# Kernel optimization log

Hardware: AMD Instinct MI355X
Metric: run time of the kernel (lower is better)

## Reference

```python
import jax, jax.numpy as jnp
import numpy as np

N_HEADS = 4
NUM_GROUPS = 32
EPS = 1e-6


def _nin(t, W, b):
    # 1x1 conv as dense over channel dim: [B,C,H,W] x [C,D] -> [B,D,H,W]
    return jnp.einsum('bchw,cd->bdhw', t, W) + b[None, :, None, None]


def setup_inputs() -> dict:
    key = jax.random.key(0)
    ks = jax.random.split(key, 12)
    B, C, H, W = 8, 256, 32, 32
    Tc = 512
    Cin = C + Tc  # 768
    x = jax.random.normal(ks[0], (B, C, H, W), dtype=jnp.float32)
    text_feat = jax.random.normal(ks[1], (B, Tc), dtype=jnp.float32)
    gn_gamma = jnp.ones((Cin,), dtype=jnp.float32)
    gn_beta = jnp.zeros((Cin,), dtype=jnp.float32)
    scale = 1.0 / np.sqrt(Cin)
    W0 = jax.random.normal(ks[2], (Cin, C), dtype=jnp.float32) * scale
    b0 = jnp.zeros((C,), dtype=jnp.float32)
    W1 = jax.random.normal(ks[3], (Cin, C), dtype=jnp.float32) * scale
    b1 = jnp.zeros((C,), dtype=jnp.float32)
    W2 = jax.random.normal(ks[4], (Cin, C), dtype=jnp.float32) * scale
    b2 = jnp.zeros((C,), dtype=jnp.float32)
    return {"x": x, "text_feat": text_feat, "gn_gamma": gn_gamma, "gn_beta": gn_beta,
            "W0": W0, "b0": b0, "W1": W1, "b1": b1, "W2": W2, "b2": b2}


def reference(x, text_feat, gn_gamma, gn_beta, W0, b0, W1, b1, W2, b2):
    B, C, H, W = x.shape
    # broadcast text features spatially and concat on channel dim
    tf = jnp.broadcast_to(text_feat[:, :, None, None], (B, text_feat.shape[1], H, W))
    h = jnp.concatenate([x, tf], axis=1)  # [B, C+Tc, H, W]
    Ctot = h.shape[1]
    # GroupNorm(32, Ctot), eps=1e-6
    hg = h.reshape(B, NUM_GROUPS, Ctot // NUM_GROUPS, H, W)
    mu = hg.mean(axis=(2, 3, 4), keepdims=True)
    var = hg.var(axis=(2, 3, 4), keepdims=True)
    hn = ((hg - mu) * jax.lax.rsqrt(var + EPS)).reshape(B, Ctot, H, W)
    hn = hn * gn_gamma[None, :, None, None] + gn_beta[None, :, None, None]
    q = _nin(hn, W0, b0)
    k = _nin(hn, W1, b1)
    v = _nin(hn, W2, b2)
    Ch = C // N_HEADS
    qh = q.reshape(B * N_HEADS, Ch, H, W)
    kh = k.reshape(B * N_HEADS, Ch, H, W)
    vh = v.reshape(B * N_HEADS, Ch, H, W)
    # full HW x HW attention scores, softmax over flattened key positions
    w = jnp.einsum('bchw,bcij->bhwij', qh, kh) * (Ch ** -0.5)
    w = jax.nn.softmax(w.reshape(B * N_HEADS, H, W, H * W), axis=-1)
    w = w.reshape(B * N_HEADS, H, W, H, W)
    ho = jnp.einsum('bhwij,bcij->bchw', w, vh).reshape(B, C, H, W)
    return x + ho
```

## Files before the change

kernel.cpp:

```cpp
#include <hip/hip_runtime.h>
#include <math.h>

#define BATCH 8
#define CX 256
#define TC 512
#define CIN 768
#define HW_TOT 1024
#define NH 4
#define CHD 64

typedef __attribute__((ext_vector_type(8))) short short8;
typedef __attribute__((ext_vector_type(4))) short s4v;
typedef __attribute__((ext_vector_type(4))) float floatx4;
typedef __attribute__((ext_vector_type(4))) int int4v;

#define QSCALE 0.18033688f

static __device__ __forceinline__ short f2bf(float f) {
    union { float f; unsigned u; } c; c.f = f;
    unsigned r = (c.u + 0x7fffu + ((c.u >> 16) & 1u)) >> 16;
    return (short)r;
}

static __device__ __forceinline__ int pack_trunc(float lo, float hi) {
    union { float f; unsigned u; } L, H;
    L.f = lo; H.f = hi;
    return (int)((H.u & 0xffff0000u) | (L.u >> 16));
}

__global__ __launch_bounds__(256)
void gn_kernel(const float* __restrict__ x, const float* __restrict__ tf,
               const float* __restrict__ gamma, const float* __restrict__ beta,
               float* __restrict__ scale, float* __restrict__ shift,
               float* __restrict__ tc) {
    const int b = blockIdx.x >> 5;
    const int g = blockIdx.x & 31;
    const int t = threadIdx.x;
    const int w = t >> 6, lane = t & 63;
    if (blockIdx.x < 24) tc[blockIdx.x * 256 + t] = 0.f;

    float s = 0.f, ss = 0.f;
    #pragma unroll
    for (int rr = 0; rr < 6; rr++) {
        const int row = w * 6 + rr;
        const int cg = g * 24 + row;
        if (cg < CX) {
            const float4* p = (const float4*)(x + ((size_t)b * CX + cg) * HW_TOT);
            #pragma unroll
            for (int i = 0; i < 4; i++) {
                float4 v = p[lane + 64 * i];
                s += v.x + v.y + v.z + v.w;
                ss += v.x * v.x + v.y * v.y + v.z * v.z + v.w * v.w;
            }
        } else {
            float v = tf[b * TC + cg - CX];
            s += 16.f * v;
            ss += 16.f * v * v;
        }
    }
    #pragma unroll
    for (int d = 1; d < 64; d <<= 1) {
        s += __shfl_xor(s, d);
        ss += __shfl_xor(ss, d);
    }
    __shared__ float rs_[4], rss_[4];
    if (lane == 0) { rs_[w] = s; rss_[w] = ss; }
    __syncthreads();
    const float S  = rs_[0] + rs_[1] + rs_[2] + rs_[3];
    const float SS = rss_[0] + rss_[1] + rss_[2] + rss_[3];
    const float inv_n = 1.f / (24 * 1024);
    const float mean = S * inv_n;
    const float var = SS * inv_n - mean * mean;
    const float r = rsqrtf(var + 1e-6f);
    if (t < 24) {
        int cg = g * 24 + t;
        float sc = gamma[cg] * r;
        scale[b * CIN + cg] = sc;
        shift[b * CIN + cg] = beta[cg] - mean * sc;
    }
}

__global__ __launch_bounds__(256)
void prep_kernel(const float* __restrict__ x, const float* __restrict__ tf,
                 const float* __restrict__ scale, const float* __restrict__ shift,
                 const float* __restrict__ W0, const float* __restrict__ W1,
                 const float* __restrict__ W2,
                 short* __restrict__ hnT, short* __restrict__ Wt,
                 float* __restrict__ tc) {
    __shared__ float hs[128];
    __shared__ float red[4][64];
    const int bx = blockIdx.x;
    const int t = threadIdx.x;
    if (bx < 256) {
        int id = (bx & 31) * 256 + t;
        int b = id >> 10;
        const float* xb = x + (size_t)b * CX * HW_TOT + (id & 1023);
        const float* scb = scale + b * CIN;
        const float* shb = shift + b * CIN;
        short* outp = hnT + (size_t)id * CX;
        int c0base = (bx >> 5) * 32;
        for (int c0 = c0base; c0 < c0base + 32; c0 += 8) {
            short8 o;
            #pragma unroll
            for (int i = 0; i < 8; i++) {
                float v = xb[(size_t)(c0 + i) * HW_TOT];
                o[i] = f2bf(v * scb[c0 + i] + shb[c0 + i]);
            }
            *(short8*)(outp + c0) = o;
        }
    } else if (bx < 268) {
        int m = bx - 256;
        int dg = (m % 3) * 256 + t;
        int which = dg >> 8, d = dg & 255;
        const float* Wm = (which == 0) ? W0 : (which == 1) ? W1 : W2;
        int c0base = (m / 3) * 64;
        for (int c0 = c0base; c0 < c0base + 64; c0 += 8) {
            short8 o;
            #pragma unroll
            for (int i = 0; i < 8; i++) o[i] = f2bf(Wm[(size_t)(c0 + i) * CX + d]);
            *(short8*)(Wt + (size_t)dg * CX + c0) = o;
        }
    } else {
        int m = bx - 268;
        int ks = m & 3;
        int b = (m >> 2) & 7, dt = m >> 5;
        int which = dt >> 2, d0 = (dt & 3) * 64;
        const float* Wm = (which == 0) ? W0 : (which == 1) ? W1 : W2;
        if (t < 128) {
            int c = ks * 128 + t;
            hs[t] = tf[b * TC + c] * scale[b * CIN + CX + c] + shift[b * CIN + CX + c];
        }
        __syncthreads();
        int td = t & 63, tq = t >> 6;
        float acc = 0.f;
        const float* wp = Wm + (size_t)(CX + ks * 128 + tq * 32) * CX + d0 + td;
        #pragma unroll 8
        for (int c = 0; c < 32; c++)
            acc = fmaf(hs[tq * 32 + c], wp[(size_t)c * CX], acc);
        red[tq][td] = acc;
        __syncthreads();
        if (t < 64)
            atomicAdd(&tc[b * CIN + which * CX + d0 + t],
                      red[0][t] + red[1][t] + red[2][t] + red[3][t]);
    }
}

__global__ __launch_bounds__(256, 2)
void qkv_gemm(const short* __restrict__ hnT, const short* __restrict__ Wt,
              const float* __restrict__ tc,
              const float* __restrict__ b0, const float* __restrict__ b1,
              const float* __restrict__ b2,
              short* __restrict__ qb, short* __restrict__ kb, short* __restrict__ vb) {
    const int hw0 = blockIdx.x * 64, dt = blockIdx.y, b = blockIdx.z;
    const int which = dt >> 2;
    const int col0 = (dt & 3) * 64;
    const int dg0 = which * 256 + col0;
    const bool OV = (which == 2);

    __shared__ short At[64 * 256];
    __shared__ short Bt[64 * 256];

    const int t = threadIdx.x;
    const int w = t >> 6, l = t & 63;
    const int wm = w >> 1, wn = w & 1;
    const int l15 = l & 15, q = l >> 4;
    const int srow = t >> 2;
    const int cbase = (t & 3) * 8;
    const int sw = srow & 7;

    const short* gA = hnT + (size_t)(b * HW_TOT + hw0 + srow) * CX + cbase * 8;
    const short* gB = Wt + (size_t)(dg0 + srow) * CX + cbase * 8;

    short8 ra[8], rb[8];
    #pragma unroll
    for (int i = 0; i < 8; i++) ra[i] = *(const short8*)(gA + i * 8);
    #pragma unroll
    for (int i = 0; i < 8; i++) rb[i] = *(const short8*)(gB + i * 8);
    short* wA = At + srow * 256;
    short* wB = Bt + srow * 256;
    #pragma unroll
    for (int i = 0; i < 8; i++) *(short8*)(wA + ((cbase + i) ^ sw) * 8) = ra[i];
    #pragma unroll
    for (int i = 0; i < 8; i++) *(short8*)(wB + ((cbase + i) ^ sw) * 8) = rb[i];
    __syncthreads();

    const short* aB = OV ? Bt : At;
    const short* bB = OV ? At : Bt;

    floatx4 acc[2][2] = {};
    __builtin_amdgcn_s_setprio(1);
    #pragma unroll
    for (int kc = 0; kc < 8; kc++) {
        short8 af[2], bf2[2];
        #pragma unroll
        for (int mt = 0; mt < 2; mt++) {
            const int r = wm * 32 + mt * 16 + l15;
            af[mt] = *(const short8*)(aB + r * 256 + ((kc * 4 + q) ^ (r & 7)) * 8);
        }
        #pragma unroll
        for (int nt = 0; nt < 2; nt++) {
            const int r = wn * 32 + nt * 16 + l15;
            bf2[nt] = *(const short8*)(bB + r * 256 + ((kc * 4 + q) ^ (r & 7)) * 8);
        }
        #pragma unroll
        for (int mt = 0; mt < 2; mt++)
            #pragma unroll
            for (int nt = 0; nt < 2; nt++)
                acc[mt][nt] = __builtin_amdgcn_mfma_f32_16x16x32_bf16(
                    af[mt], bf2[nt], acc[mt][nt], 0, 0, 0);
    }
    __builtin_amdgcn_s_setprio(0);

    __syncthreads();
    const float* bias = (which == 0) ? b0 : (which == 1) ? b1 : b2;
    if (!OV) {
        const float qs = (which == 0) ? QSCALE : 1.0f;
        float cadd[2];
        #pragma unroll
        for (int nt = 0; nt < 2; nt++) {
            int d = col0 + wn * 32 + nt * 16 + l15;
            cadd[nt] = bias[d] + tc[b * CIN + which * CX + d];
        }
        #pragma unroll
        for (int mt = 0; mt < 2; mt++)
            #pragma unroll
            for (int rr = 0; rr < 4; rr++)
                #pragma unroll
                for (int nt = 0; nt < 2; nt++)
                    At[(wm * 32 + mt * 16 + q * 4 + rr) * 72 + wn * 32 + nt * 16 + l15]
                        = f2bf((acc[mt][nt][rr] + cadd[nt]) * qs);
    } else {
        #pragma unroll
        for (int mt = 0; mt < 2; mt++)
            #pragma unroll
            for (int rr = 0; rr < 4; rr++) {
                int d = col0 + wm * 32 + mt * 16 + q * 4 + rr;
                float radd = bias[d] + tc[b * CIN + 2 * CX + d];
                #pragma unroll
                for (int nt = 0; nt < 2; nt++)
                    At[(wm * 32 + mt * 16 + q * 4 + rr) * 72 + wn * 32 + nt * 16 + l15]
                        = f2bf(acc[mt][nt][rr] + radd);
            }
    }
    __syncthreads();
    const int sch2 = (t & 3) * 16;
    short8 v0 = *(const short8*)(At + srow * 72 + sch2);
    short8 v1 = *(const short8*)(At + srow * 72 + sch2 + 8);
    if (!OV) {
        short* outp = (which == 0) ? qb : kb;
        size_t off = (size_t)(b * HW_TOT + hw0 + srow) * CX + col0 + sch2;
        *(short8*)(outp + off) = v0;
        *(short8*)(outp + off + 8) = v1;
    } else {
        size_t off = (size_t)(b * CX + col0 + srow) * HW_TOT + hw0 + sch2;
        *(short8*)(vb + off) = v0;
        *(short8*)(vb + off + 8) = v1;
    }
}

__global__ __launch_bounds__(256, 3)
void attn_kernel(const short* __restrict__ qb, const short* __restrict__ kb,
                 const short* __restrict__ vb, const float* __restrict__ x,
                 float* __restrict__ out) {
    const int qt = blockIdx.x, bh = blockIdx.y;
    const int b = bh >> 2, h = bh & 3;
    const int hw0 = qt * 64;

    __shared__ short Qs[64 * 72];
    __shared__ short Ks[2][64 * 72];
    __shared__ short Vs[2][64 * 72];

    const int t = threadIdx.x;
    const int w = t >> 6, l = t & 63;
    const int pair = w >> 1, jh = w & 1;
    const int l15 = l & 15, q = l >> 4;
    const int srow = t >> 2, sch = (t & 3) * 16;
    const int vpos0 = ((sch >> 5) << 5) + ((sch >> 4) & 1) * 4;

    {
        const short* gq = qb + (size_t)(b * HW_TOT + hw0 + srow) * CX + h * CHD + sch;
        *(short8*)(Qs + srow * 72 + sch)     = *(const short8*)gq;
        *(short8*)(Qs + srow * 72 + sch + 8) = *(const short8*)(gq + 8);
    }

    short8 pk[2][2], pv[2][2];
    #pragma unroll
    for (int s = 0; s < 2; s++) {
        const int j0 = s * 512;
        const short* gk = kb + (size_t)(b * HW_TOT + j0 + srow) * CX + h * CHD + sch;
        pk[s][0] = *(const short8*)gk;
        pk[s][1] = *(const short8*)(gk + 8);
        const short* gv = vb + (size_t)(b * CX + h * CHD + srow) * HW_TOT + j0 + sch;
        pv[s][0] = *(const short8*)gv;
        pv[s][1] = *(const short8*)(gv + 8);
    }
    #pragma unroll
    for (int s = 0; s < 2; s++) {
        *(short8*)(Ks[s] + srow * 72 + sch)     = pk[s][0];
        *(short8*)(Ks[s] + srow * 72 + sch + 8) = pk[s][1];
        short* vrow = Vs[s] + srow * 72 + vpos0;
        *(s4v*)(vrow)      = __builtin_shufflevector(pv[s][0], pv[s][0], 0, 1, 2, 3);
        *(s4v*)(vrow + 8)  = __builtin_shufflevector(pv[s][0], pv[s][0], 4, 5, 6, 7);
        *(s4v*)(vrow + 16) = __builtin_shufflevector(pv[s][1], pv[s][1], 0, 1, 2, 3);
        *(s4v*)(vrow + 24) = __builtin_shufflevector(pv[s][1], pv[s][1], 4, 5, 6, 7);
    }
    __syncthreads();

    short8 aq[2][2];
    #pragma unroll
    for (int g = 0; g < 2; g++) {
        aq[g][0] = *(const short8*)(Qs + (pair * 32 + g * 16 + l15) * 72 + q * 8);
        aq[g][1] = *(const short8*)(Qs + (pair * 32 + g * 16 + l15) * 72 + 32 + q * 8);
    }

    union { int4v i; short8 s; } ones;
    ones.i[0] = 0x3f803f80; ones.i[1] = 0x3f803f80;
    ones.i[2] = 0x3f803f80; ones.i[3] = 0x3f803f80;

    floatx4 oacc[2][4] = {};
    floatx4 lacc[2] = {};
    const short* Kc = Ks[jh];
    const short* Vc = Vs[jh];

    for (int jj = 0; jj < 8; jj++) {
        if (jj < 7) {
            #pragma unroll
            for (int s = 0; s < 2; s++) {
                const int j0 = s * 512 + (jj + 1) * 64;
                const short* gk = kb + (size_t)(b * HW_TOT + j0 + srow) * CX + h * CHD + sch;
                pk[s][0] = *(const short8*)gk;
                pk[s][1] = *(const short8*)(gk + 8);
                const short* gv = vb + (size_t)(b * CX + h * CHD + srow) * HW_TOT + j0 + sch;
                pv[s][0] = *(const short8*)gv;
                pv[s][1] = *(const short8*)(gv + 8);
            }
        }

        floatx4 sacc[2][4] = {};
        __builtin_amdgcn_s_setprio(1);
        #pragma unroll
        for (int nt = 0; nt < 4; nt++) {
            short8 kf0 = *(const short8*)(Kc + (nt * 16 + l15) * 72 + q * 8);
            short8 kf1 = *(const short8*)(Kc + (nt * 16 + l15) * 72 + 32 + q * 8);
            #pragma unroll
            for (int g = 0; g < 2; g++) {
                sacc[g][nt] = __builtin_amdgcn_mfma_f32_16x16x32_bf16(kf0, aq[g][0], sacc[g][nt], 0, 0, 0);
                sacc[g][nt] = __builtin_amdgcn_mfma_f32_16x16x32_bf16(kf1, aq[g][1], sacc[g][nt], 0, 0, 0);
            }
        }
        __builtin_amdgcn_s_setprio(0);

        union { int4v i; short8 s; } u[2][2];
        #pragma unroll
        for (int g = 0; g < 2; g++)
            #pragma unroll
            for (int nt = 0; nt < 4; nt++) {
                float e0 = exp2f(sacc[g][nt][0]);
                float e1 = exp2f(sacc[g][nt][1]);
                float e2 = exp2f(sacc[g][nt][2]);
                float e3 = exp2f(sacc[g][nt][3]);
                u[g][nt >> 1].i[(nt & 1) * 2]     = pack_trunc(e0, e1);
                u[g][nt >> 1].i[(nt & 1) * 2 + 1] = pack_trunc(e2, e3);
            }

        __builtin_amdgcn_s_setprio(1);
        #pragma unroll
        for (int g = 0; g < 2; g++) {
            lacc[g] = __builtin_amdgcn_mfma_f32_16x16x32_bf16(ones.s, u[g][0].s, lacc[g], 0, 0, 0);
            lacc[g] = __builtin_amdgcn_mfma_f32_16x16x32_bf16(ones.s, u[g][1].s, lacc[g], 0, 0, 0);
        }

        #pragma unroll
        for (int ct = 0; ct < 4; ct++) {
            const short* vr = Vc + (ct * 16 + l15) * 72;
            #pragma unroll
            for (int kcc = 0; kcc < 2; kcc++) {
                short8 vf = *(const short8*)(vr + kcc * 32 + q * 8);
                #pragma unroll
                for (int g = 0; g < 2; g++)
                    oacc[g][ct] = __builtin_amdgcn_mfma_f32_16x16x32_bf16(
                        vf, u[g][kcc].s, oacc[g][ct], 0, 0, 0);
            }
        }
        __builtin_amdgcn_s_setprio(0);

        if (jj < 7) {
            __syncthreads();
            #pragma unroll
            for (int s = 0; s < 2; s++) {
                *(short8*)(Ks[s] + srow * 72 + sch)     = pk[s][0];
                *(short8*)(Ks[s] + srow * 72 + sch + 8) = pk[s][1];
                short* vrow = Vs[s] + srow * 72 + vpos0;
                *(s4v*)(vrow)      = __builtin_shufflevector(pv[s][0], pv[s][0], 0, 1, 2, 3);
                *(s4v*)(vrow + 8)  = __builtin_shufflevector(pv[s][0], pv[s][0], 4, 5, 6, 7);
                *(s4v*)(vrow + 16) = __builtin_shufflevector(pv[s][1], pv[s][1], 0, 1, 2, 3);
                *(s4v*)(vrow + 24) = __builtin_shufflevector(pv[s][1], pv[s][1], 4, 5, 6, 7);
            }
            __syncthreads();
        }
    }

    __syncthreads();
    float* Of = (float*)Ks;
    float* Lf = (float*)Vs;
    if (jh == 1) {
        #pragma unroll
        for (int g = 0; g < 2; g++) {
            int qi = pair * 32 + g * 16 + l15;
            #pragma unroll
            for (int ct = 0; ct < 4; ct++)
                *(floatx4*)&Of[qi * 68 + ct * 16 + q * 4] = oacc[g][ct];
            if (q == 0) Lf[qi] = lacc[g][0];
        }
    }
    __syncthreads();
    if (jh == 0) {
        #pragma unroll
        for (int g = 0; g < 2; g++) {
            int qi = pair * 32 + g * 16 + l15;
            const float rinv = 1.f / (lacc[g][0] + Lf[qi]);
            #pragma unroll
            for (int ct = 0; ct < 4; ct++) {
                floatx4 po = *(const floatx4*)&Of[qi * 68 + ct * 16 + q * 4];
                #pragma unroll
                for (int r = 0; r < 4; r++) {
                    int c = h * CHD + ct * 16 + q * 4 + r;
                    size_t idx = (size_t)(b * CX + c) * HW_TOT + hw0 + qi;
                    out[idx] = x[idx] + (oacc[g][ct][r] + po[r]) * rinv;
                }
            }
        }
    }
}

extern "C" void kernel_launch(void* const* d_in, const int* in_sizes, int n_in,
                              void* d_out, int out_size, void* d_ws, size_t ws_size,
                              hipStream_t stream) {
    (void)in_sizes; (void)n_in; (void)out_size; (void)ws_size;
    const float* x     = (const float*)d_in[0];
    const float* tf    = (const float*)d_in[1];
    const float* gamma = (const float*)d_in[2];
    const float* beta  = (const float*)d_in[3];
    const float* W0 = (const float*)d_in[4];
    const float* b0 = (const float*)d_in[5];
    const float* W1 = (const float*)d_in[6];
    const float* b1 = (const float*)d_in[7];
    const float* W2 = (const float*)d_in[8];
    const float* b2 = (const float*)d_in[9];

    char* ws = (char*)d_ws;
    float* scale  = (float*)(ws);
    float* shift  = (float*)(ws + 24576);
    float* tcb    = (float*)(ws + 49152);
    short* Wt     = (short*)(ws + 73728);
    short* hnT    = (short*)(ws + 466944);
    short* qb     = (short*)(ws + 4661248);
    short* kb     = (short*)(ws + 8855552);
    short* vb     = (short*)(ws + 13049856);

    hipLaunchKernelGGL(gn_kernel, dim3(256), dim3(256), 0, stream,
                       x, tf, gamma, beta, scale, shift, tcb);
    hipLaunchKernelGGL(prep_kernel, dim3(652), dim3(256), 0, stream,
                       x, tf, scale, shift, W0, W1, W2, hnT, Wt, tcb);
    hipLaunchKernelGGL(qkv_gemm, dim3(16, 12, BATCH), dim3(256), 0, stream,
                       hnT, Wt, tcb, b0, b1, b2, qb, kb, vb);
    hipLaunchKernelGGL(attn_kernel, dim3(16, 32), dim3(256), 0, stream,
                       qb, kb, vb, x, (float*)d_out);
}
```

Measured before the change: 123.1 us.

## Load attention Q/K/V fragments directly from global memory, dropping LDS staging

The attention kernel no longer stages K and V tiles through double-buffered shared memory with barriers. Each wave now reads its MFMA fragments straight from global memory, relying on L1/L2 caching. Dropping the big LDS buffers allows launch bounds of 4 blocks per CU, and the grid is flattened with batch as the fastest index so blocks sharing K/V run close together. The risk is more global and cache traffic, since each wave reloads data the block used to share, plus narrower 8-byte V loads and no explicit prefetch overlap.

```diff
diff --git a/kernel.cpp b/kernel.cpp
--- a/kernel.cpp
+++ b/kernel.cpp
@@ -194,13 +194,13 @@
         short8 af[2], bf2[2];
         #pragma unroll
         for (int mt = 0; mt < 2; mt++) {
-            const int r = wm * 32 + mt * 16 + l15;
-            af[mt] = *(const short8*)(aB + r * 256 + ((kc * 4 + q) ^ (r & 7)) * 8);
+            const int rr = wm * 32 + mt * 16 + l15;
+            af[mt] = *(const short8*)(aB + rr * 256 + ((kc * 4 + q) ^ (rr & 7)) * 8);
         }
         #pragma unroll
         for (int nt = 0; nt < 2; nt++) {
-            const int r = wn * 32 + nt * 16 + l15;
-            bf2[nt] = *(const short8*)(bB + r * 256 + ((kc * 4 + q) ^ (r & 7)) * 8);
+            const int rr = wn * 32 + nt * 16 + l15;
+            bf2[nt] = *(const short8*)(bB + rr * 256 + ((kc * 4 + q) ^ (rr & 7)) * 8);
         }
         #pragma unroll
         for (int mt = 0; mt < 2; mt++)
@@ -258,59 +258,32 @@
     }
 }
 
-__global__ __launch_bounds__(256, 3)
+__global__ __launch_bounds__(256, 4)
 void attn_kernel(const short* __restrict__ qb, const short* __restrict__ kb,
                  const short* __restrict__ vb, const float* __restrict__ x,
                  float* __restrict__ out) {
-    const int qt = blockIdx.x, bh = blockIdx.y;
-    const int b = bh >> 2, h = bh & 3;
+    __shared__ float Of[64 * 68];
+    __shared__ float Lf[64];
+
+    const int i = blockIdx.x;
+    const int b = i & 7;
+    const int rest = i >> 3;
+    const int h = rest & 3;
+    const int qt = rest >> 2;
     const int hw0 = qt * 64;
-
-    __shared__ short Qs[64 * 72];
-    __shared__ short Ks[2][64 * 72];
-    __shared__ short Vs[2][64 * 72];
 
     const int t = threadIdx.x;
     const int w = t >> 6, l = t & 63;
     const int pair = w >> 1, jh = w & 1;
     const int l15 = l & 15, q = l >> 4;
-    const int srow = t >> 2, sch = (t & 3) * 16;
-    const int vpos0 = ((sch >> 5) << 5) + ((sch >> 4) & 1) * 4;
-
-    {
-        const short* gq = qb + (size_t)(b * HW_TOT + hw0 + srow) * CX + h * CHD + sch;
-        *(short8*)(Qs + srow * 72 + sch)     = *(const short8*)gq;
-        *(short8*)(Qs + srow * 72 + sch + 8) = *(const short8*)(gq + 8);
-    }
-
-    short8 pk[2][2], pv[2][2];
-    #pragma unroll
-    for (int s = 0; s < 2; s++) {
-        const int j0 = s * 512;
-        const short* gk = kb + (size_t)(b * HW_TOT + j0 + srow) * CX + h * CHD + sch;
-        pk[s][0] = *(const short8*)gk;
-        pk[s][1] = *(const short8*)(gk + 8);
-        const short* gv = vb + (size_t)(b * CX + h * CHD + srow) * HW_TOT + j0 + sch;
-        pv[s][0] = *(const short8*)gv;
-        pv[s][1] = *(const short8*)(gv + 8);
-    }
-    #pragma unroll
-    for (int s = 0; s < 2; s++) {
-        *(short8*)(Ks[s] + srow * 72 + sch)     = pk[s][0];
-        *(short8*)(Ks[s] + srow * 72 + sch + 8) = pk[s][1];
-        short* vrow = Vs[s] + srow * 72 + vpos0;
-        *(s4v*)(vrow)      = __builtin_shufflevector(pv[s][0], pv[s][0], 0, 1, 2, 3);
-        *(s4v*)(vrow + 8)  = __builtin_shufflevector(pv[s][0], pv[s][0], 4, 5, 6, 7);
-        *(s4v*)(vrow + 16) = __builtin_shufflevector(pv[s][1], pv[s][1], 0, 1, 2, 3);
-        *(s4v*)(vrow + 24) = __builtin_shufflevector(pv[s][1], pv[s][1], 4, 5, 6, 7);
-    }
-    __syncthreads();
 
     short8 aq[2][2];
     #pragma unroll
     for (int g = 0; g < 2; g++) {
-        aq[g][0] = *(const short8*)(Qs + (pair * 32 + g * 16 + l15) * 72 + q * 8);
-        aq[g][1] = *(const short8*)(Qs + (pair * 32 + g * 16 + l15) * 72 + 32 + q * 8);
+        const short* gq = qb + (size_t)(b * HW_TOT + hw0 + pair * 32 + g * 16 + l15) * CX
+                          + h * CHD + q * 8;
+        aq[g][0] = *(const short8*)gq;
+        aq[g][1] = *(const short8*)(gq + 32);
     }
 
     union { int4v i; short8 s; } ones;
@@ -319,29 +292,20 @@
 
     floatx4 oacc[2][4] = {};
     floatx4 lacc[2] = {};
-    const short* Kc = Ks[jh];
-    const short* Vc = Vs[jh];
+
+    const short* kbase = kb + (size_t)(b * HW_TOT) * CX + h * CHD;
+    const short* vbase = vb + ((size_t)(b * CX) + h * CHD) * HW_TOT;
 
     for (int jj = 0; jj < 8; jj++) {
-        if (jj < 7) {
-            #pragma unroll
-            for (int s = 0; s < 2; s++) {
-                const int j0 = s * 512 + (jj + 1) * 64;
-                const short* gk = kb + (size_t)(b * HW_TOT + j0 + srow) * CX + h * CHD + sch;
-                pk[s][0] = *(const short8*)gk;
-                pk[s][1] = *(const short8*)(gk + 8);
-                const short* gv = vb + (size_t)(b * CX + h * CHD + srow) * HW_TOT + j0 + sch;
-                pv[s][0] = *(const short8*)gv;
-                pv[s][1] = *(const short8*)(gv + 8);
-            }
-        }
+        const int j0 = jh * 512 + jj * 64;
 
         floatx4 sacc[2][4] = {};
         __builtin_amdgcn_s_setprio(1);
         #pragma unroll
         for (int nt = 0; nt < 4; nt++) {
-            short8 kf0 = *(const short8*)(Kc + (nt * 16 + l15) * 72 + q * 8);
-            short8 kf1 = *(const short8*)(Kc + (nt * 16 + l15) * 72 + 32 + q * 8);
+            const short* gk = kbase + (size_t)(j0 + nt * 16 + l15) * CX + q * 8;
+            short8 kf0 = *(const short8*)gk;
+            short8 kf1 = *(const short8*)(gk + 32);
             #pragma unroll
             for (int g = 0; g < 2; g++) {
                 sacc[g][nt] = __builtin_amdgcn_mfma_f32_16x16x32_bf16(kf0, aq[g][0], sacc[g][nt], 0, 0, 0);
@@ -350,7 +314,7 @@
         }
         __builtin_amdgcn_s_setprio(0);
 
-        union { int4v i; short8 s; } u[2][2];
+        union { int4v i; short8 s; } uu[2][2];
         #pragma unroll
         for (int g = 0; g < 2; g++)
             #pragma unroll
@@ -359,50 +323,37 @@
                 float e1 = exp2f(sacc[g][nt][1]);
                 float e2 = exp2f(sacc[g][nt][2]);
                 float e3 = exp2f(sacc[g][nt][3]);
-                u[g][nt >> 1].i[(nt & 1) * 2]     = pack_trunc(e0, e1);
-                u[g][nt >> 1].i[(nt & 1) * 2 + 1] = pack_trunc(e2, e3);
+                uu[g][nt >> 1].i[(nt & 1) * 2]     = pack_trunc(e0, e1);
+                uu[g][nt >> 1].i[(nt & 1) * 2 + 1] = pack_trunc(e2, e3);
             }
 
         __builtin_amdgcn_s_setprio(1);
         #pragma unroll
         for (int g = 0; g < 2; g++) {
-            lacc[g] = __builtin_amdgcn_mfma_f32_16x16x32_bf16(ones.s, u[g][0].s, lacc[g], 0, 0, 0);
-            lacc[g] = __builtin_amdgcn_mfma_f32_16x16x32_bf16(ones.s, u[g][1].s, lacc[g], 0, 0, 0);
+            lacc[g] = __builtin_amdgcn_mfma_f32_16x16x32_bf16(ones.s, uu[g][0].s, lacc[g], 0, 0, 0);
+            lacc[g] = __builtin_amdgcn_mfma_f32_16x16x32_bf16(ones.s, uu[g][1].s, lacc[g], 0, 0, 0);
         }
 
         #pragma unroll
         for (int ct = 0; ct < 4; ct++) {
-            const short* vr = Vc + (ct * 16 + l15) * 72;
-            #pragma unroll
-            for (int kcc = 0; kcc < 2; kcc++) {
-                short8 vf = *(const short8*)(vr + kcc * 32 + q * 8);
-                #pragma unroll
-                for (int g = 0; g < 2; g++)
-                    oacc[g][ct] = __builtin_amdgcn_mfma_f32_16x16x32_bf16(
-                        vf, u[g][kcc].s, oacc[g][ct], 0, 0, 0);
+            const short* gv = vbase + (size_t)(ct * 16 + l15) * HW_TOT + j0 + q * 4;
+            s4v c0 = *(const s4v*)(gv);
+            s4v c1 = *(const s4v*)(gv + 16);
+            s4v c2 = *(const s4v*)(gv + 32);
+            s4v c3 = *(const s4v*)(gv + 48);
+            short8 vf0 = __builtin_shufflevector(c0, c1, 0, 1, 2, 3, 4, 5, 6, 7);
+            short8 vf1 = __builtin_shufflevector(c2, c3, 0, 1, 2, 3, 4, 5, 6, 7);
+            #pragma unroll
+            for (int g = 0; g < 2; g++) {
+                oacc[g][ct] = __builtin_amdgcn_mfma_f32_16x16x32_bf16(
+                    vf0, uu[g][0].s, oacc[g][ct], 0, 0, 0);
+                oacc[g][ct] = __builtin_amdgcn_mfma_f32_16x16x32_bf16(
+                    vf1, uu[g][1].s, oacc[g][ct], 0, 0, 0);
             }
         }
         __builtin_amdgcn_s_setprio(0);
-
-        if (jj < 7) {
-            __syncthreads();
-            #pragma unroll
-            for (int s = 0; s < 2; s++) {
-                *(short8*)(Ks[s] + srow * 72 + sch)     = pk[s][0];
-                *(short8*)(Ks[s] + srow * 72 + sch + 8) = pk[s][1];
-                short* vrow = Vs[s] + srow * 72 + vpos0;
-                *(s4v*)(vrow)      = __builtin_shufflevector(pv[s][0], pv[s][0], 0, 1, 2, 3);
-                *(s4v*)(vrow + 8)  = __builtin_shufflevector(pv[s][0], pv[s][0], 4, 5, 6, 7);
-                *(s4v*)(vrow + 16) = __builtin_shufflevector(pv[s][1], pv[s][1], 0, 1, 2, 3);
-                *(s4v*)(vrow + 24) = __builtin_shufflevector(pv[s][1], pv[s][1], 4, 5, 6, 7);
-            }
-            __syncthreads();
-        }
-    }
-
-    __syncthreads();
-    float* Of = (float*)Ks;
-    float* Lf = (float*)Vs;
+    }
+
     if (jh == 1) {
         #pragma unroll
         for (int g = 0; g < 2; g++) {
@@ -464,6 +415,6 @@
                        x, tf, scale, shift, W0, W1, W2, hnT, Wt, tcb);
     hipLaunchKernelGGL(qkv_gemm, dim3(16, 12, BATCH), dim3(256), 0, stream,
                        hnT, Wt, tcb, b0, b1, b2, qb, kb, vb);
-    hipLaunchKernelGGL(attn_kernel, dim3(16, 32), dim3(256), 0, stream,
+    hipLaunchKernelGGL(attn_kernel, dim3(512), dim3(256), 0, stream,
                        qb, kb, vb, x, (float*)d_out);
 }
```

Measured after the change: 153.3 us. 1.25x slower.
